# Kernel optimization log

Hardware: AMD Instinct MI355X
Metric: run time of the kernel (lower is better)

Reference implementation:

```python
import jax, jax.numpy as jnp
import numpy as np

EPS = 1e-05

def setup_inputs() -> dict:
    key = jax.random.key(0)
    k1, k2, k3 = jax.random.split(key, 3)
    B, S, D_IN, D_OUT = 4, 2048, 4096, 12288
    x = jax.random.normal(k1, (B, S, D_IN), dtype=jnp.float32)
    weight = jax.random.normal(k2, (D_OUT, D_IN), dtype=jnp.float32) * (1.0 / np.sqrt(D_IN))
    bias = jnp.zeros((D_OUT,), dtype=jnp.float32)
    ln_weight = jnp.ones((D_IN,), dtype=jnp.float32)
    ln_bias = jnp.zeros((D_IN,), dtype=jnp.float32)
    return {"x": x, "weight": weight, "bias": bias, "ln_weight": ln_weight, "ln_bias": ln_bias}

def reference(x, weight, bias, ln_weight, ln_bias):
    # LayerNorm over last dim
    mean = jnp.mean(x, axis=-1, keepdims=True)
    var = jnp.mean(jnp.square(x - mean), axis=-1, keepdims=True)
    normed = (x - mean) * jax.lax.rsqrt(var + EPS) * ln_weight + ln_bias
    # Linear: y = normed @ W^T + b
    return jnp.einsum('bsd,od->bso', normed, weight) + bias
```

## Files before the change

kernel.cpp:

```cpp
#include <hip/hip_runtime.h>
#include <hip/hip_bf16.h>
#include <stdint.h>

typedef __attribute__((ext_vector_type(8))) short short8_t;
typedef __attribute__((ext_vector_type(4))) float f32x4;

__device__ __forceinline__ unsigned short f2bf(float f) {
  union { float f; unsigned int u; } a;
  a.f = f;
  unsigned int u = a.u;
  u += 0x7fffu + ((u >> 16) & 1u);
  return (unsigned short)(u >> 16);
}

__device__ __forceinline__ void gload_lds16(const void* g, void* l) {
  __builtin_amdgcn_global_load_lds(
      (const __attribute__((address_space(1))) void*)g,
      (__attribute__((address_space(3))) void*)l, 16, 0, 0);
}

constexpr int D_IN = 4096;

__global__ __launch_bounds__(256) void ln_bf16_kernel(
    const float* __restrict__ x, const float* __restrict__ lnw,
    const float* __restrict__ lnb, unsigned short* __restrict__ out) {
  const int row = blockIdx.x;
  const int tid = threadIdx.x;
  const float* xr = x + (size_t)row * D_IN;

  f32x4 v[4];
  float sum = 0.f, sq = 0.f;
#pragma unroll
  for (int i = 0; i < 4; ++i) {
    v[i] = __builtin_nontemporal_load(
        reinterpret_cast<const f32x4*>(xr + i * 1024 + tid * 4));
    sum += v[i][0] + v[i][1] + v[i][2] + v[i][3];
    sq += v[i][0]*v[i][0] + v[i][1]*v[i][1] + v[i][2]*v[i][2] + v[i][3]*v[i][3];
  }
#pragma unroll
  for (int off = 32; off > 0; off >>= 1) {
    sum += __shfl_down(sum, off, 64);
    sq  += __shfl_down(sq, off, 64);
  }
  __shared__ float s_sum[4], s_sq[4];
  if ((tid & 63) == 0) { s_sum[tid >> 6] = sum; s_sq[tid >> 6] = sq; }
  __syncthreads();
  const float fs = s_sum[0] + s_sum[1] + s_sum[2] + s_sum[3];
  const float fq = s_sq[0] + s_sq[1] + s_sq[2] + s_sq[3];
  const float mean = fs * (1.f / D_IN);
  const float var = fq * (1.f / D_IN) - mean * mean;
  const float rstd = rsqrtf(var + 1e-5f);

  unsigned short* orow = out + (size_t)row * D_IN;
#pragma unroll
  for (int i = 0; i < 4; ++i) {
    const int col = i * 1024 + tid * 4;
    const f32x4 w = *reinterpret_cast<const f32x4*>(lnw + col);
    const f32x4 b = *reinterpret_cast<const f32x4*>(lnb + col);
    ushort4 o;
    o.x = f2bf((v[i][0] - mean) * rstd * w[0] + b[0]);
    o.y = f2bf((v[i][1] - mean) * rstd * w[1] + b[1]);
    o.z = f2bf((v[i][2] - mean) * rstd * w[2] + b[2]);
    o.w = f2bf((v[i][3] - mean) * rstd * w[3] + b[3]);
    *reinterpret_cast<ushort4*>(orow + col) = o;
  }
}

__global__ __launch_bounds__(256) void f32_to_bf16_kernel(
    const float* __restrict__ in, unsigned short* __restrict__ out) {
  const size_t i = ((size_t)blockIdx.x * 256 + threadIdx.x) * 8;
  const f32x4 a = __builtin_nontemporal_load(reinterpret_cast<const f32x4*>(in + i));
  const f32x4 b = __builtin_nontemporal_load(reinterpret_cast<const f32x4*>(in + i + 4));
  ushort4 lo, hi;
  lo.x = f2bf(a[0]); lo.y = f2bf(a[1]); lo.z = f2bf(a[2]); lo.w = f2bf(a[3]);
  hi.x = f2bf(b[0]); hi.y = f2bf(b[1]); hi.z = f2bf(b[2]); hi.w = f2bf(b[3]);
  *reinterpret_cast<ushort4*>(out + i) = lo;
  *reinterpret_cast<ushort4*>(out + i + 4) = hi;
}


#define RD(P, IMM) (*reinterpret_cast<const short8_t*>((P) + (IMM)))

#define READ8(S, KK)                                                \
  _Pragma("unroll") for (int m_ = 0; m_ < 4; ++m_)                  \
    af[m_] = RD((KK) ? aB1 : aB0, (S)*32768 + m_*2048);             \
  _Pragma("unroll") for (int n_ = 0; n_ < 4; ++n_)                  \
    bfr[n_] = RD((KK) ? bB1 : bB0, (S)*32768 + n_*2048);

#define MFMA16                                                      \
  _Pragma("unroll") for (int m_ = 0; m_ < 4; ++m_) {                \
    _Pragma("unroll") for (int n_ = 0; n_ < 4; ++n_)                \
      acc[m_][n_] = __builtin_amdgcn_mfma_f32_16x16x32_bf16(        \
          af[m_], bfr[n_], acc[m_][n_], 0, 0, 0);                   \
  }

#define STAGE_A(S, U, KT) \
  gload_lds16(aSrc + (size_t)((U)*128) * K + (size_t)(KT)*64, ldsAw + (S)*32768 + (U)*16384)
#define STAGE_B(S, U, KT) \
  gload_lds16(bSrc + (size_t)((U)*128) * K + (size_t)(KT)*64, ldsBw + (S)*32768 + (U)*16384)
#define STAGE_ALL(S, KT)                                            \
  STAGE_A(S,0,KT); STAGE_A(S,1,KT); STAGE_B(S,0,KT); STAGE_B(S,1,KT);

#define XREG(S)                                                     \
  READ8(S, 0)                                                       \
  __builtin_amdgcn_s_setprio(1);                                    \
  MFMA16                                                            \
  READ8(S, 1)                                                       \
  __builtin_amdgcn_s_setprio(0);                                    \
  asm volatile("s_waitcnt lgkmcnt(0)" ::: "memory");                \
  __builtin_amdgcn_s_barrier();                                     \
  asm volatile("" ::: "memory");

#define YREG(S, KT)                                                 \
  STAGE_ALL(S, KT)                                                  \
  __builtin_amdgcn_s_setprio(1);                                    \
  MFMA16                                                            \
  __builtin_amdgcn_s_setprio(0);                                    \
  asm volatile("s_waitcnt vmcnt(4)" ::: "memory");                  \
  __builtin_amdgcn_s_barrier();                                     \
  asm volatile("" ::: "memory");

__global__ __launch_bounds__(1024, 4) void gemm_xy16(
    const unsigned short* __restrict__ A,
    const unsigned short* __restrict__ B,
    const float* __restrict__ bias,
    float* __restrict__ C,
    int M, int N, int K, int NYB, int BXP) {
  extern __shared__ char smem[];
  const int tid = threadIdx.x;
  const int lane = tid & 63;
  const int wid = tid >> 6;
  const int wr = wid >> 2, wc = wid & 3;
  const int fr = lane & 15;
  const int q16 = (lane >> 4) * 16;

  const int id = blockIdx.x;
  const int xcd = id & 7;
  const int s = id >> 3;
  const int gsz = 8 * BXP;
  const int g = s / gsz;
  const int j = s - g * gsz;
  const int by = g * 8 + (j & 7);
  const int bx = xcd * BXP + (j >> 3);
  const int m0 = by * 256, n0 = bx * 256;

  const int s_log = (tid * 16) ^ (((tid >> 3) & 7) << 4);
  const int rsw = s_log >> 7;
  const int csw = (s_log & 127) >> 1;
  const unsigned short* aSrc = A + (size_t)(m0 + rsw) * K + csw;
  const unsigned short* bSrc = B + (size_t)(n0 + rsw) * K + csw;

  char* const ldsAw = smem + wid * 1024;
  char* const ldsBw = smem + 65536 + wid * 1024;

  const int s7 = (fr & 7) << 4;
  const char* const aB0 = smem + (wr * 64 + fr) * 128 + (q16 ^ s7);
  const char* const aB1 = smem + (wr * 64 + fr) * 128 + ((64 + q16) ^ s7);
  const char* const bB0 = smem + 65536 + (wc * 64 + fr) * 128 + (q16 ^ s7);
  const char* const bB1 = smem + 65536 + (wc * 64 + fr) * 128 + ((64 + q16) ^ s7);

  f32x4 acc[4][4] = {};
  short8_t af[4], bfr[4];

  STAGE_ALL(0, 0)
  STAGE_ALL(1, 1)
  asm volatile("s_waitcnt vmcnt(4)" ::: "memory");
  __builtin_amdgcn_s_barrier();
  asm volatile("" ::: "memory");

  const int NK = K >> 6;
  for (int t = 0; t < (NK - 2) >> 1; ++t) {
    const int k2 = 2*t + 2, k3 = 2*t + 3;
    XREG(0) YREG(0, k2)
    XREG(1) YREG(1, k3)
  }
  {
    READ8(0, 0)
    __builtin_amdgcn_s_setprio(1);
    MFMA16
    READ8(0, 1)
    MFMA16
    __builtin_amdgcn_s_setprio(0);
    asm volatile("s_waitcnt lgkmcnt(0)\n\ts_waitcnt vmcnt(0)" ::: "memory");
    __builtin_amdgcn_s_barrier();
    asm volatile("" ::: "memory");
    READ8(1, 0)
    __builtin_amdgcn_s_setprio(1);
    MFMA16
    READ8(1, 1)
    MFMA16
    __builtin_amdgcn_s_setprio(0);
  }

  __syncthreads();
  float* const buf = (float*)smem;
  const int cr = (lane >> 4) * 4;
  float bv[4];
#pragma unroll
  for (int ni = 0; ni < 4; ++ni) bv[ni] = bias[n0 + wc * 64 + ni * 16 + fr];

#pragma unroll
  for (int half = 0; half < 4; ++half) {
    if (wr == half) {
#pragma unroll
      for (int mi = 0; mi < 4; ++mi) {
#pragma unroll
        for (int jj = 0; jj < 4; ++jj) {
          const int lr = mi * 16 + cr + jj;
#pragma unroll
          for (int ni = 0; ni < 4; ++ni)
            buf[lr * 260 + wc * 64 + ni * 16 + fr] = acc[mi][ni][jj] + bv[ni];
        }
      }
    }
    __syncthreads();
#pragma unroll
    for (int i = 0; i < 4; ++i) {
      const int idx = wid * 4 + i;
      const f32x4 vv = *reinterpret_cast<const f32x4*>(buf + idx * 260 + lane * 4);
      const int grow = m0 + half * 64 + idx;
      __builtin_nontemporal_store(
          vv, reinterpret_cast<f32x4*>(C + (size_t)grow * N + n0) + lane);
    }
    __syncthreads();
  }
}

extern "C" void kernel_launch(void* const* d_in, const int* in_sizes, int n_in,
                              void* d_out, int out_size, void* d_ws, size_t ws_size,
                              hipStream_t stream) {
  const float* x    = (const float*)d_in[0];
  const float* w    = (const float*)d_in[1];
  const float* bias = (const float*)d_in[2];
  const float* lnw  = (const float*)d_in[3];
  const float* lnb  = (const float*)d_in[4];
  float* out = (float*)d_out;

  const int DIN  = 4096;
  const int M    = in_sizes[0] / DIN;
  const int DOUT = in_sizes[2];

  unsigned short* normA = (unsigned short*)d_ws;
  unsigned short* wB    = normA + (size_t)M * DIN;

  ln_bf16_kernel<<<M, 256, 0, stream>>>(x, lnw, lnb, normA);
  f32_to_bf16_kernel<<<((size_t)DOUT * DIN) / (256 * 8), 256, 0, stream>>>(w, wB);

  const int nwg = (M / 256) * (DOUT / 256);
  (void)hipFuncSetAttribute((const void*)gemm_xy16,
                            hipFuncAttributeMaxDynamicSharedMemorySize, 131072);
  gemm_xy16<<<nwg, 1024, 131072, stream>>>(normA, wB, bias, out,
                                           M, DOUT, DIN, M / 256, (DOUT / 256) / 8);
}
```

Baseline: 757.1 us.

## Switch GEMM to 8 waves with 128x64 per-wave tiles and register double-buffering

The GEMM block drops from 16 waves to 8. Each wave now computes a 128x64 sub-tile with 8x4 MFMA accumulators. LDS fragments are double-buffered in two register sets (afA/bfA and afB/bfB), so the next half-K reads overlap the current MFMAs. Global-to-LDS staging issues 8 loads per thread per stage and now waits with vmcnt(0). This targets better MFMA-to-LDS-read ratio and latency hiding, at the cost of much higher register pressure (128 accumulator VGPRs plus 24 fragment registers) and fewer waves to hide latency. The epilogue is restructured to write two 64-row halves at once.

```diff
diff --git a/kernel.cpp b/kernel.cpp
--- a/kernel.cpp
+++ b/kernel.cpp
@@ -81,46 +81,45 @@
 
 #define RD(P, IMM) (*reinterpret_cast<const short8_t*>((P) + (IMM)))
 
-#define READ8(S, KK)                                                \
-  _Pragma("unroll") for (int m_ = 0; m_ < 4; ++m_)                  \
-    af[m_] = RD((KK) ? aB1 : aB0, (S)*32768 + m_*2048);             \
+#define READ12(S, KK, AF, BF)                                       \
+  _Pragma("unroll") for (int m_ = 0; m_ < 8; ++m_)                  \
+    AF[m_] = RD((KK) ? aB1 : aB0, (S)*32768 + m_*2048);             \
   _Pragma("unroll") for (int n_ = 0; n_ < 4; ++n_)                  \
-    bfr[n_] = RD((KK) ? bB1 : bB0, (S)*32768 + n_*2048);
-
-#define MFMA16                                                      \
-  _Pragma("unroll") for (int m_ = 0; m_ < 4; ++m_) {                \
+    BF[n_] = RD((KK) ? bB1 : bB0, (S)*32768 + n_*2048);
+
+#define MFMA32(AF, BF)                                              \
+  _Pragma("unroll") for (int m_ = 0; m_ < 8; ++m_) {                \
     _Pragma("unroll") for (int n_ = 0; n_ < 4; ++n_)                \
       acc[m_][n_] = __builtin_amdgcn_mfma_f32_16x16x32_bf16(        \
-          af[m_], bfr[n_], acc[m_][n_], 0, 0, 0);                   \
+          AF[m_], BF[n_], acc[m_][n_], 0, 0, 0);                    \
   }
 
 #define STAGE_A(S, U, KT) \
-  gload_lds16(aSrc + (size_t)((U)*128) * K + (size_t)(KT)*64, ldsAw + (S)*32768 + (U)*16384)
+  gload_lds16(aSrc + (size_t)((U)*64) * K + (size_t)(KT)*64, ldsAw + (S)*32768 + (U)*8192)
 #define STAGE_B(S, U, KT) \
-  gload_lds16(bSrc + (size_t)((U)*128) * K + (size_t)(KT)*64, ldsBw + (S)*32768 + (U)*16384)
+  gload_lds16(bSrc + (size_t)((U)*64) * K + (size_t)(KT)*64, ldsBw + (S)*32768 + (U)*8192)
 #define STAGE_ALL(S, KT)                                            \
-  STAGE_A(S,0,KT); STAGE_A(S,1,KT); STAGE_B(S,0,KT); STAGE_B(S,1,KT);
-
-#define XREG(S)                                                     \
-  READ8(S, 0)                                                       \
+  STAGE_A(S,0,KT); STAGE_A(S,1,KT); STAGE_A(S,2,KT); STAGE_A(S,3,KT); \
+  STAGE_B(S,0,KT); STAGE_B(S,1,KT); STAGE_B(S,2,KT); STAGE_B(S,3,KT);
+
+#define REGION(S, KT2)                                              \
+  asm volatile("s_waitcnt vmcnt(0)" ::: "memory");                  \
+  __builtin_amdgcn_s_barrier();                                     \
+  asm volatile("" ::: "memory");                                    \
+  READ12(S, 1, afB, bfB)                                            \
   __builtin_amdgcn_s_setprio(1);                                    \
-  MFMA16                                                            \
-  READ8(S, 1)                                                       \
+  MFMA32(afA, bfA)                                                  \
   __builtin_amdgcn_s_setprio(0);                                    \
   asm volatile("s_waitcnt lgkmcnt(0)" ::: "memory");                \
   __builtin_amdgcn_s_barrier();                                     \
-  asm volatile("" ::: "memory");
-
-#define YREG(S, KT)                                                 \
-  STAGE_ALL(S, KT)                                                  \
+  asm volatile("" ::: "memory");                                    \
+  STAGE_ALL(S, KT2)                                                 \
+  READ12(1-(S), 0, afA, bfA)                                        \
   __builtin_amdgcn_s_setprio(1);                                    \
-  MFMA16                                                            \
-  __builtin_amdgcn_s_setprio(0);                                    \
-  asm volatile("s_waitcnt vmcnt(4)" ::: "memory");                  \
-  __builtin_amdgcn_s_barrier();                                     \
-  asm volatile("" ::: "memory");
-
-__global__ __launch_bounds__(1024, 4) void gemm_xy16(
+  MFMA32(afB, bfB)                                                  \
+  __builtin_amdgcn_s_setprio(0);
+
+__global__ __launch_bounds__(512, 2) void gemm_pipe(
     const unsigned short* __restrict__ A,
     const unsigned short* __restrict__ B,
     const float* __restrict__ bias,
@@ -154,71 +153,78 @@
   char* const ldsBw = smem + 65536 + wid * 1024;
 
   const int s7 = (fr & 7) << 4;
-  const char* const aB0 = smem + (wr * 64 + fr) * 128 + (q16 ^ s7);
-  const char* const aB1 = smem + (wr * 64 + fr) * 128 + ((64 + q16) ^ s7);
+  const char* const aB0 = smem + (wr * 128 + fr) * 128 + (q16 ^ s7);
+  const char* const aB1 = smem + (wr * 128 + fr) * 128 + ((64 + q16) ^ s7);
   const char* const bB0 = smem + 65536 + (wc * 64 + fr) * 128 + (q16 ^ s7);
   const char* const bB1 = smem + 65536 + (wc * 64 + fr) * 128 + ((64 + q16) ^ s7);
 
-  f32x4 acc[4][4] = {};
-  short8_t af[4], bfr[4];
+  f32x4 acc[8][4] = {};
+  short8_t afA[8], bfA[4];
+  short8_t afB[8], bfB[4];
 
   STAGE_ALL(0, 0)
   STAGE_ALL(1, 1)
-  asm volatile("s_waitcnt vmcnt(4)" ::: "memory");
+  asm volatile("s_waitcnt vmcnt(8)" ::: "memory");
   __builtin_amdgcn_s_barrier();
   asm volatile("" ::: "memory");
+  READ12(0, 0, afA, bfA)
 
   const int NK = K >> 6;
   for (int t = 0; t < (NK - 2) >> 1; ++t) {
-    const int k2 = 2*t + 2, k3 = 2*t + 3;
-    XREG(0) YREG(0, k2)
-    XREG(1) YREG(1, k3)
+    REGION(0, 2*t + 2)
+    REGION(1, 2*t + 3)
   }
   {
-    READ8(0, 0)
-    __builtin_amdgcn_s_setprio(1);
-    MFMA16
-    READ8(0, 1)
-    MFMA16
-    __builtin_amdgcn_s_setprio(0);
-    asm volatile("s_waitcnt lgkmcnt(0)\n\ts_waitcnt vmcnt(0)" ::: "memory");
+    asm volatile("s_waitcnt vmcnt(0)" ::: "memory");
     __builtin_amdgcn_s_barrier();
     asm volatile("" ::: "memory");
-    READ8(1, 0)
+    READ12(0, 1, afB, bfB)
     __builtin_amdgcn_s_setprio(1);
-    MFMA16
-    READ8(1, 1)
-    MFMA16
+    MFMA32(afA, bfA)
     __builtin_amdgcn_s_setprio(0);
+    asm volatile("s_waitcnt lgkmcnt(0)" ::: "memory");
+    __builtin_amdgcn_s_barrier();
+    asm volatile("" ::: "memory");
+    READ12(1, 0, afA, bfA)
+    __builtin_amdgcn_s_setprio(1);
+    MFMA32(afB, bfB)
+    __builtin_amdgcn_s_setprio(0);
+    READ12(1, 1, afB, bfB)
+    __builtin_amdgcn_s_setprio(1);
+    MFMA32(afA, bfA)
+    MFMA32(afB, bfB)
+    __builtin_amdgcn_s_setprio(0);
   }
 
   __syncthreads();
-  float* const buf = (float*)smem;
+  float* const buf0 = (float*)smem;
+  float* const buf1 = (float*)smem + 64 * 260;
   const int cr = (lane >> 4) * 4;
   float bv[4];
 #pragma unroll
   for (int ni = 0; ni < 4; ++ni) bv[ni] = bias[n0 + wc * 64 + ni * 16 + fr];
 
 #pragma unroll
-  for (int half = 0; half < 4; ++half) {
-    if (wr == half) {
-#pragma unroll
-      for (int mi = 0; mi < 4; ++mi) {
-#pragma unroll
-        for (int jj = 0; jj < 4; ++jj) {
-          const int lr = mi * 16 + cr + jj;
-#pragma unroll
-          for (int ni = 0; ni < 4; ++ni)
-            buf[lr * 260 + wc * 64 + ni * 16 + fr] = acc[mi][ni][jj] + bv[ni];
-        }
+  for (int half = 0; half < 2; ++half) {
+    float* const wbuf = (wr == 0) ? buf0 : buf1;
+#pragma unroll
+    for (int mi4 = 0; mi4 < 4; ++mi4) {
+      const int mi = half * 4 + mi4;
+#pragma unroll
+      for (int jj = 0; jj < 4; ++jj) {
+        const int lr = mi4 * 16 + cr + jj;
+#pragma unroll
+        for (int ni = 0; ni < 4; ++ni)
+          wbuf[lr * 260 + wc * 64 + ni * 16 + fr] = acc[mi][ni][jj] + bv[ni];
       }
     }
     __syncthreads();
 #pragma unroll
-    for (int i = 0; i < 4; ++i) {
-      const int idx = wid * 4 + i;
-      const f32x4 vv = *reinterpret_cast<const f32x4*>(buf + idx * 260 + lane * 4);
-      const int grow = m0 + half * 64 + idx;
+    for (int i = 0; i < 16; ++i) {
+      const int idx = wid * 16 + i;
+      const float* src = (idx < 64 ? buf0 + idx * 260 : buf1 + (idx - 64) * 260) + lane * 4;
+      const int grow = m0 + (idx < 64 ? half * 64 + idx : 128 + half * 64 + (idx - 64));
+      const f32x4 vv = *reinterpret_cast<const f32x4*>(src);
       __builtin_nontemporal_store(
           vv, reinterpret_cast<f32x4*>(C + (size_t)grow * N + n0) + lane);
     }
@@ -247,8 +253,9 @@
   f32_to_bf16_kernel<<<((size_t)DOUT * DIN) / (256 * 8), 256, 0, stream>>>(w, wB);
 
   const int nwg = (M / 256) * (DOUT / 256);
-  (void)hipFuncSetAttribute((const void*)gemm_xy16,
-                            hipFuncAttributeMaxDynamicSharedMemorySize, 131072);
-  gemm_xy16<<<nwg, 1024, 131072, stream>>>(normA, wB, bias, out,
-                                           M, DOUT, DIN, M / 256, (DOUT / 256) / 8);
-}
+  const int smem_bytes = 2 * 64 * 260 * 4 > 131072 ? 2 * 64 * 260 * 4 : 131072;
+  (void)hipFuncSetAttribute((const void*)gemm_pipe,
+                            hipFuncAttributeMaxDynamicSharedMemorySize, 163840);
+  gemm_pipe<<<nwg, 512, smem_bytes, stream>>>(normA, wB, bias, out,
+                                              M, DOUT, DIN, M / 256, (DOUT / 256) / 8);
+}
```

New measurement: 1.072 ms. 1.42x slower.

## Shrink GEMM tile to 128x128 with 512 threads and direct epilogue stores

Applied to the files above, without the earlier changes.

Reduces the GEMM workgroup tile from 256x256 (16 waves) to 128x128 (8 waves). Each wave now computes 64x32 instead of 64x64, and LDS use halves to 64KB. The LDS-staged coalesced epilogue is replaced with direct per-element nontemporal stores from the accumulators. The smaller tile lowers operand reuse and raises global/L2 traffic. The epilogue stores become scalar and only partly coalesced, in exchange for more workgroups and fewer barriers.

```diff
diff --git a/kernel.cpp b/kernel.cpp
--- a/kernel.cpp
+++ b/kernel.cpp
@@ -81,31 +81,31 @@
 
 #define RD(P, IMM) (*reinterpret_cast<const short8_t*>((P) + (IMM)))
 
-#define READ8(S, KK)                                                \
+#define READ6(S, KK)                                                \
   _Pragma("unroll") for (int m_ = 0; m_ < 4; ++m_)                  \
-    af[m_] = RD((KK) ? aB1 : aB0, (S)*32768 + m_*2048);             \
-  _Pragma("unroll") for (int n_ = 0; n_ < 4; ++n_)                  \
-    bfr[n_] = RD((KK) ? bB1 : bB0, (S)*32768 + n_*2048);
-
-#define MFMA16                                                      \
+    af[m_] = RD((KK) ? aB1 : aB0, (S)*16384 + m_*2048);             \
+  _Pragma("unroll") for (int n_ = 0; n_ < 2; ++n_)                  \
+    bfr[n_] = RD((KK) ? bB1 : bB0, (S)*16384 + n_*2048);
+
+#define MFMA8                                                       \
   _Pragma("unroll") for (int m_ = 0; m_ < 4; ++m_) {                \
-    _Pragma("unroll") for (int n_ = 0; n_ < 4; ++n_)                \
+    _Pragma("unroll") for (int n_ = 0; n_ < 2; ++n_)                \
       acc[m_][n_] = __builtin_amdgcn_mfma_f32_16x16x32_bf16(        \
           af[m_], bfr[n_], acc[m_][n_], 0, 0, 0);                   \
   }
 
 #define STAGE_A(S, U, KT) \
-  gload_lds16(aSrc + (size_t)((U)*128) * K + (size_t)(KT)*64, ldsAw + (S)*32768 + (U)*16384)
+  gload_lds16(aSrc + (size_t)((U)*64) * K + (size_t)(KT)*64, ldsAw + (S)*16384 + (U)*8192)
 #define STAGE_B(S, U, KT) \
-  gload_lds16(bSrc + (size_t)((U)*128) * K + (size_t)(KT)*64, ldsBw + (S)*32768 + (U)*16384)
+  gload_lds16(bSrc + (size_t)((U)*64) * K + (size_t)(KT)*64, ldsBw + (S)*16384 + (U)*8192)
 #define STAGE_ALL(S, KT)                                            \
   STAGE_A(S,0,KT); STAGE_A(S,1,KT); STAGE_B(S,0,KT); STAGE_B(S,1,KT);
 
 #define XREG(S)                                                     \
-  READ8(S, 0)                                                       \
+  READ6(S, 0)                                                       \
   __builtin_amdgcn_s_setprio(1);                                    \
-  MFMA16                                                            \
-  READ8(S, 1)                                                       \
+  MFMA8                                                             \
+  READ6(S, 1)                                                       \
   __builtin_amdgcn_s_setprio(0);                                    \
   asm volatile("s_waitcnt lgkmcnt(0)" ::: "memory");                \
   __builtin_amdgcn_s_barrier();                                     \
@@ -114,13 +114,13 @@
 #define YREG(S, KT)                                                 \
   STAGE_ALL(S, KT)                                                  \
   __builtin_amdgcn_s_setprio(1);                                    \
-  MFMA16                                                            \
+  MFMA8                                                             \
   __builtin_amdgcn_s_setprio(0);                                    \
   asm volatile("s_waitcnt vmcnt(4)" ::: "memory");                  \
   __builtin_amdgcn_s_barrier();                                     \
   asm volatile("" ::: "memory");
 
-__global__ __launch_bounds__(1024, 4) void gemm_xy16(
+__global__ __launch_bounds__(512, 4) void gemm_xy128(
     const unsigned short* __restrict__ A,
     const unsigned short* __restrict__ B,
     const float* __restrict__ bias,
@@ -142,7 +142,7 @@
   const int j = s - g * gsz;
   const int by = g * 8 + (j & 7);
   const int bx = xcd * BXP + (j >> 3);
-  const int m0 = by * 256, n0 = bx * 256;
+  const int m0 = by * 128, n0 = bx * 128;
 
   const int s_log = (tid * 16) ^ (((tid >> 3) & 7) << 4);
   const int rsw = s_log >> 7;
@@ -151,16 +151,16 @@
   const unsigned short* bSrc = B + (size_t)(n0 + rsw) * K + csw;
 
   char* const ldsAw = smem + wid * 1024;
-  char* const ldsBw = smem + 65536 + wid * 1024;
+  char* const ldsBw = smem + 32768 + wid * 1024;
 
   const int s7 = (fr & 7) << 4;
   const char* const aB0 = smem + (wr * 64 + fr) * 128 + (q16 ^ s7);
   const char* const aB1 = smem + (wr * 64 + fr) * 128 + ((64 + q16) ^ s7);
-  const char* const bB0 = smem + 65536 + (wc * 64 + fr) * 128 + (q16 ^ s7);
-  const char* const bB1 = smem + 65536 + (wc * 64 + fr) * 128 + ((64 + q16) ^ s7);
-
-  f32x4 acc[4][4] = {};
-  short8_t af[4], bfr[4];
+  const char* const bB0 = smem + 32768 + (wc * 32 + fr) * 128 + (q16 ^ s7);
+  const char* const bB1 = smem + 32768 + (wc * 32 + fr) * 128 + ((64 + q16) ^ s7);
+
+  f32x4 acc[4][2] = {};
+  short8_t af[4], bfr[2];
 
   STAGE_ALL(0, 0)
   STAGE_ALL(1, 1)
@@ -170,59 +170,41 @@
 
   const int NK = K >> 6;
   for (int t = 0; t < (NK - 2) >> 1; ++t) {
-    const int k2 = 2*t + 2, k3 = 2*t + 3;
-    XREG(0) YREG(0, k2)
-    XREG(1) YREG(1, k3)
+    XREG(0) YREG(0, 2*t + 2)
+    XREG(1) YREG(1, 2*t + 3)
   }
   {
-    READ8(0, 0)
+    READ6(0, 0)
     __builtin_amdgcn_s_setprio(1);
-    MFMA16
-    READ8(0, 1)
-    MFMA16
+    MFMA8
+    READ6(0, 1)
+    MFMA8
     __builtin_amdgcn_s_setprio(0);
     asm volatile("s_waitcnt lgkmcnt(0)\n\ts_waitcnt vmcnt(0)" ::: "memory");
     __builtin_amdgcn_s_barrier();
     asm volatile("" ::: "memory");
-    READ8(1, 0)
+    READ6(1, 0)
     __builtin_amdgcn_s_setprio(1);
-    MFMA16
-    READ8(1, 1)
-    MFMA16
+    MFMA8
+    READ6(1, 1)
+    MFMA8
     __builtin_amdgcn_s_setprio(0);
   }
 
-  __syncthreads();
-  float* const buf = (float*)smem;
-  const int cr = (lane >> 4) * 4;
-  float bv[4];
-#pragma unroll
-  for (int ni = 0; ni < 4; ++ni) bv[ni] = bias[n0 + wc * 64 + ni * 16 + fr];
-
-#pragma unroll
-  for (int half = 0; half < 4; ++half) {
-    if (wr == half) {
-#pragma unroll
-      for (int mi = 0; mi < 4; ++mi) {
-#pragma unroll
-        for (int jj = 0; jj < 4; ++jj) {
-          const int lr = mi * 16 + cr + jj;
-#pragma unroll
-          for (int ni = 0; ni < 4; ++ni)
-            buf[lr * 260 + wc * 64 + ni * 16 + fr] = acc[mi][ni][jj] + bv[ni];
-        }
-      }
+  const int fq = lane >> 4;
+  float bv[2];
+#pragma unroll
+  for (int n = 0; n < 2; ++n) bv[n] = bias[n0 + wc * 32 + n * 16 + fr];
+#pragma unroll
+  for (int m = 0; m < 4; ++m) {
+#pragma unroll
+    for (int jj = 0; jj < 4; ++jj) {
+      const int row = m0 + wr * 64 + m * 16 + fq * 4 + jj;
+      float* Crow = C + (size_t)row * N + n0 + wc * 32 + fr;
+#pragma unroll
+      for (int n = 0; n < 2; ++n)
+        __builtin_nontemporal_store(acc[m][n][jj] + bv[n], Crow + n * 16);
     }
-    __syncthreads();
-#pragma unroll
-    for (int i = 0; i < 4; ++i) {
-      const int idx = wid * 4 + i;
-      const f32x4 vv = *reinterpret_cast<const f32x4*>(buf + idx * 260 + lane * 4);
-      const int grow = m0 + half * 64 + idx;
-      __builtin_nontemporal_store(
-          vv, reinterpret_cast<f32x4*>(C + (size_t)grow * N + n0) + lane);
-    }
-    __syncthreads();
   }
 }
 
@@ -246,9 +228,9 @@
   ln_bf16_kernel<<<M, 256, 0, stream>>>(x, lnw, lnb, normA);
   f32_to_bf16_kernel<<<((size_t)DOUT * DIN) / (256 * 8), 256, 0, stream>>>(w, wB);
 
-  const int nwg = (M / 256) * (DOUT / 256);
-  (void)hipFuncSetAttribute((const void*)gemm_xy16,
-                            hipFuncAttributeMaxDynamicSharedMemorySize, 131072);
-  gemm_xy16<<<nwg, 1024, 131072, stream>>>(normA, wB, bias, out,
-                                           M, DOUT, DIN, M / 256, (DOUT / 256) / 8);
-}
+  const int nwg = (M / 128) * (DOUT / 128);
+  (void)hipFuncSetAttribute((const void*)gemm_xy128,
+                            hipFuncAttributeMaxDynamicSharedMemorySize, 65536);
+  gemm_xy128<<<nwg, 512, 65536, stream>>>(normA, wB, bias, out,
+                                          M, DOUT, DIN, M / 128, (DOUT / 128) / 8);
+}
```

Measured after the change: 813.4 us. 7.4% more time.

## Shrink GEMM tile to 256x128 with single-buffered A and direct epilogue stores

Applied to the files above, without the earlier changes.

Replaces the 256x256, 1024-thread GEMM with a 256x128 tile on 512 threads using 64KB LDS. A is kept in a single LDS buffer while B stays double-buffered, and the prefetch schedule is reworked to match. The LDS-staged coalesced epilogue is replaced by direct per-element nontemporal stores from registers. The aim is higher occupancy and fewer barriers, at the cost of re-reading A twice as often, less reuse per tile, and uncoalesced scalar output stores.

```diff
diff --git a/kernel.cpp b/kernel.cpp
--- a/kernel.cpp
+++ b/kernel.cpp
@@ -83,9 +83,9 @@
 
 #define READ8(S, KK)                                                \
   _Pragma("unroll") for (int m_ = 0; m_ < 4; ++m_)                  \
-    af[m_] = RD((KK) ? aB1 : aB0, (S)*32768 + m_*2048);             \
+    af[m_] = RD((KK) ? aB1 : aB0, m_*2048);                         \
   _Pragma("unroll") for (int n_ = 0; n_ < 4; ++n_)                  \
-    bfr[n_] = RD((KK) ? bB1 : bB0, (S)*32768 + n_*2048);
+    bfr[n_] = RD((KK) ? bB1 : bB0, (S)*16384 + n_*2048);
 
 #define MFMA16                                                      \
   _Pragma("unroll") for (int m_ = 0; m_ < 4; ++m_) {                \
@@ -94,33 +94,36 @@
           af[m_], bfr[n_], acc[m_][n_], 0, 0, 0);                   \
   }
 
-#define STAGE_A(S, U, KT) \
-  gload_lds16(aSrc + (size_t)((U)*128) * K + (size_t)(KT)*64, ldsAw + (S)*32768 + (U)*16384)
-#define STAGE_B(S, U, KT) \
-  gload_lds16(bSrc + (size_t)((U)*128) * K + (size_t)(KT)*64, ldsBw + (S)*32768 + (U)*16384)
-#define STAGE_ALL(S, KT)                                            \
-  STAGE_A(S,0,KT); STAGE_A(S,1,KT); STAGE_B(S,0,KT); STAGE_B(S,1,KT);
+#define STAGE_A4(KT)                                                \
+  gload_lds16(aSrc + (size_t)(KT)*64,                 ldsAw);           \
+  gload_lds16(aSrc + (size_t)64*K  + (size_t)(KT)*64, ldsAw + 8192);    \
+  gload_lds16(aSrc + (size_t)128*K + (size_t)(KT)*64, ldsAw + 16384);   \
+  gload_lds16(aSrc + (size_t)192*K + (size_t)(KT)*64, ldsAw + 24576);
+#define STAGE_B2(S, KT)                                             \
+  gload_lds16(bSrc + (size_t)(KT)*64,                ldsBw + (S)*16384);        \
+  gload_lds16(bSrc + (size_t)64*K + (size_t)(KT)*64, ldsBw + (S)*16384 + 8192);
 
 #define XREG(S)                                                     \
   READ8(S, 0)                                                       \
   __builtin_amdgcn_s_setprio(1);                                    \
   MFMA16                                                            \
+  __builtin_amdgcn_s_setprio(0);                                    \
   READ8(S, 1)                                                       \
-  __builtin_amdgcn_s_setprio(0);                                    \
   asm volatile("s_waitcnt lgkmcnt(0)" ::: "memory");                \
   __builtin_amdgcn_s_barrier();                                     \
   asm volatile("" ::: "memory");
 
-#define YREG(S, KT)                                                 \
-  STAGE_ALL(S, KT)                                                  \
+#define YREG(S, KTA, KTB)                                           \
+  STAGE_A4(KTA)                                                     \
+  STAGE_B2(S, KTB)                                                  \
   __builtin_amdgcn_s_setprio(1);                                    \
   MFMA16                                                            \
   __builtin_amdgcn_s_setprio(0);                                    \
-  asm volatile("s_waitcnt vmcnt(4)" ::: "memory");                  \
+  asm volatile("s_waitcnt vmcnt(2)" ::: "memory");                  \
   __builtin_amdgcn_s_barrier();                                     \
   asm volatile("" ::: "memory");
 
-__global__ __launch_bounds__(1024, 4) void gemm_xy16(
+__global__ __launch_bounds__(512, 4) void gemm_ab(
     const unsigned short* __restrict__ A,
     const unsigned short* __restrict__ B,
     const float* __restrict__ bias,
@@ -130,7 +133,7 @@
   const int tid = threadIdx.x;
   const int lane = tid & 63;
   const int wid = tid >> 6;
-  const int wr = wid >> 2, wc = wid & 3;
+  const int wr = wid >> 1, wc = wid & 1;
   const int fr = lane & 15;
   const int q16 = (lane >> 4) * 16;
 
@@ -142,7 +145,7 @@
   const int j = s - g * gsz;
   const int by = g * 8 + (j & 7);
   const int bx = xcd * BXP + (j >> 3);
-  const int m0 = by * 256, n0 = bx * 256;
+  const int m0 = by * 256, n0 = bx * 128;
 
   const int s_log = (tid * 16) ^ (((tid >> 3) & 7) << 4);
   const int rsw = s_log >> 7;
@@ -151,78 +154,63 @@
   const unsigned short* bSrc = B + (size_t)(n0 + rsw) * K + csw;
 
   char* const ldsAw = smem + wid * 1024;
-  char* const ldsBw = smem + 65536 + wid * 1024;
+  char* const ldsBw = smem + 32768 + wid * 1024;
 
   const int s7 = (fr & 7) << 4;
   const char* const aB0 = smem + (wr * 64 + fr) * 128 + (q16 ^ s7);
   const char* const aB1 = smem + (wr * 64 + fr) * 128 + ((64 + q16) ^ s7);
-  const char* const bB0 = smem + 65536 + (wc * 64 + fr) * 128 + (q16 ^ s7);
-  const char* const bB1 = smem + 65536 + (wc * 64 + fr) * 128 + ((64 + q16) ^ s7);
+  const char* const bB0 = smem + 32768 + (wc * 64 + fr) * 128 + (q16 ^ s7);
+  const char* const bB1 = smem + 32768 + (wc * 64 + fr) * 128 + ((64 + q16) ^ s7);
 
   f32x4 acc[4][4] = {};
   short8_t af[4], bfr[4];
 
-  STAGE_ALL(0, 0)
-  STAGE_ALL(1, 1)
-  asm volatile("s_waitcnt vmcnt(4)" ::: "memory");
+  STAGE_A4(0)
+  STAGE_B2(0, 0)
+  STAGE_B2(1, 1)
+  asm volatile("s_waitcnt vmcnt(2)" ::: "memory");
   __builtin_amdgcn_s_barrier();
   asm volatile("" ::: "memory");
 
   const int NK = K >> 6;
   for (int t = 0; t < (NK - 2) >> 1; ++t) {
-    const int k2 = 2*t + 2, k3 = 2*t + 3;
-    XREG(0) YREG(0, k2)
-    XREG(1) YREG(1, k3)
+    const int k0 = 2*t, k1 = 2*t + 1;
+    XREG(0) YREG(0, k0 + 1, k0 + 2)
+    XREG(1) YREG(1, k1 + 1, k1 + 2)
   }
   {
-    READ8(0, 0)
+    XREG(0)
+    STAGE_A4(NK - 1)
     __builtin_amdgcn_s_setprio(1);
     MFMA16
-    READ8(0, 1)
-    MFMA16
     __builtin_amdgcn_s_setprio(0);
-    asm volatile("s_waitcnt lgkmcnt(0)\n\ts_waitcnt vmcnt(0)" ::: "memory");
+    asm volatile("s_waitcnt vmcnt(0)" ::: "memory");
     __builtin_amdgcn_s_barrier();
     asm volatile("" ::: "memory");
     READ8(1, 0)
     __builtin_amdgcn_s_setprio(1);
     MFMA16
+    __builtin_amdgcn_s_setprio(0);
     READ8(1, 1)
+    __builtin_amdgcn_s_setprio(1);
     MFMA16
     __builtin_amdgcn_s_setprio(0);
   }
 
-  __syncthreads();
-  float* const buf = (float*)smem;
-  const int cr = (lane >> 4) * 4;
+  const int fq = lane >> 4;
   float bv[4];
 #pragma unroll
-  for (int ni = 0; ni < 4; ++ni) bv[ni] = bias[n0 + wc * 64 + ni * 16 + fr];
-
-#pragma unroll
-  for (int half = 0; half < 4; ++half) {
-    if (wr == half) {
-#pragma unroll
-      for (int mi = 0; mi < 4; ++mi) {
-#pragma unroll
-        for (int jj = 0; jj < 4; ++jj) {
-          const int lr = mi * 16 + cr + jj;
-#pragma unroll
-          for (int ni = 0; ni < 4; ++ni)
-            buf[lr * 260 + wc * 64 + ni * 16 + fr] = acc[mi][ni][jj] + bv[ni];
-        }
-      }
+  for (int n = 0; n < 4; ++n) bv[n] = bias[n0 + wc * 64 + n * 16 + fr];
+#pragma unroll
+  for (int m = 0; m < 4; ++m) {
+#pragma unroll
+    for (int jj = 0; jj < 4; ++jj) {
+      const int row = m0 + wr * 64 + m * 16 + fq * 4 + jj;
+      float* Crow = C + (size_t)row * N + n0 + wc * 64 + fr;
+#pragma unroll
+      for (int n = 0; n < 4; ++n)
+        __builtin_nontemporal_store(acc[m][n][jj] + bv[n], Crow + n * 16);
     }
-    __syncthreads();
-#pragma unroll
-    for (int i = 0; i < 4; ++i) {
-      const int idx = wid * 4 + i;
-      const f32x4 vv = *reinterpret_cast<const f32x4*>(buf + idx * 260 + lane * 4);
-      const int grow = m0 + half * 64 + idx;
-      __builtin_nontemporal_store(
-          vv, reinterpret_cast<f32x4*>(C + (size_t)grow * N + n0) + lane);
-    }
-    __syncthreads();
   }
 }
 
@@ -246,9 +234,9 @@
   ln_bf16_kernel<<<M, 256, 0, stream>>>(x, lnw, lnb, normA);
   f32_to_bf16_kernel<<<((size_t)DOUT * DIN) / (256 * 8), 256, 0, stream>>>(w, wB);
 
-  const int nwg = (M / 256) * (DOUT / 256);
-  (void)hipFuncSetAttribute((const void*)gemm_xy16,
-                            hipFuncAttributeMaxDynamicSharedMemorySize, 131072);
-  gemm_xy16<<<nwg, 1024, 131072, stream>>>(normA, wB, bias, out,
-                                           M, DOUT, DIN, M / 256, (DOUT / 256) / 8);
-}
+  const int nwg = (M / 256) * (DOUT / 128);
+  (void)hipFuncSetAttribute((const void*)gemm_ab,
+                            hipFuncAttributeMaxDynamicSharedMemorySize, 65536);
+  gemm_ab<<<nwg, 512, 65536, stream>>>(normA, wB, bias, out,
+                                       M, DOUT, DIN, M / 256, (DOUT / 128) / 8);
+}
```

Measured after the change: 1.074 ms. 1.42x slower.
